# Performance work log

Hardware: AMD Instinct MI355X
Metric: run time of the kernel (lower is better)

The kernel has to match this reference:

```python
import jax, jax.numpy as jnp
import numpy as np

N_NODES = 100000
N_EDGES = 800000
F_IN, HID, N_CLS = 128, 512, 40
BN_EPS = 1e-5


def gcn_conv(x, W, b, src, dst, num_nodes):
    # PyG GCNConv: add self-loops, symmetric normalization.
    ones = jnp.ones(src.shape[0], x.dtype)
    deg = jax.ops.segment_sum(ones, dst, num_segments=num_nodes) + 1.0  # +1 self-loop
    dinv = jax.lax.rsqrt(deg)  # deg^-1/2, deg >= 1 so safe
    h = x @ W  # [N, out]
    norm = dinv[src] * dinv[dst]  # [E]
    agg = jax.ops.segment_sum(h[src] * norm[:, None], dst, num_segments=num_nodes)
    agg = agg + h * (dinv * dinv)[:, None]  # self-loop term: deg_i^-1 * h_i
    return agg + b


def batch_norm(x, gamma, beta):
    # training-mode BatchNorm over node axis (biased variance)
    mu = jnp.mean(x, axis=0)
    var = jnp.var(x, axis=0)
    return gamma * (x - mu) * jax.lax.rsqrt(var + BN_EPS) + beta


def setup_inputs() -> dict:
    key = jax.random.key(0)
    ks = jax.random.split(key, 12)
    x = jax.random.normal(ks[0], (N_NODES, F_IN), jnp.float32)
    edge_index = jax.random.randint(ks[1], (2, N_EDGES), 0, N_NODES, jnp.int64)
    def lin(k, fi, fo):
        s = 1.0 / np.sqrt(fi)
        return jax.random.uniform(k, (fi, fo), jnp.float32, -s, s)
    return {
        "x": x, "edge_index": edge_index,
        "W1": lin(ks[2], F_IN, HID), "b1": jnp.zeros((HID,), jnp.float32),
        "g1": jnp.ones((HID,), jnp.float32), "be1": jnp.zeros((HID,), jnp.float32),
        "W2": lin(ks[3], HID, HID), "b2": jnp.zeros((HID,), jnp.float32),
        "g2": jnp.ones((HID,), jnp.float32), "be2": jnp.zeros((HID,), jnp.float32),
        "W3": lin(ks[4], HID, N_CLS), "b3": jnp.zeros((N_CLS,), jnp.float32),
        "g3": jnp.ones((N_CLS,), jnp.float32), "be3": jnp.zeros((N_CLS,), jnp.float32),
    }


def reference(x, edge_index, W1, b1, g1, be1, W2, b2, g2, be2, W3, b3, g3, be3):
    src, dst = edge_index[0], edge_index[1]
    x1 = batch_norm(gcn_conv(x, W1, b1, src, dst, N_NODES), g1, be1)
    x3 = jax.nn.relu(x1)  # dropout is identity in eval mode
    x4 = batch_norm(gcn_conv(x3, W2, b2, src, dst, N_NODES), g2, be2)
    x6 = jax.nn.relu(x4)
    out = batch_norm(gcn_conv(x6, W3, b3, src, dst, N_NODES), g3, be3)
    return (out, x6)
```

## Files before the change

kernel.cpp:

```cpp
#include <hip/hip_runtime.h>
#include <cstddef>
#include <cstdint>


#define NN 100000
#define MPAD 100096
#define NE 800000
#define FIN 128
#define HIDD 512
#define NCLS 40
#define BN_EPS 1e-5f

typedef unsigned short ushort_t;
typedef __bf16 bf16x8_t __attribute__((ext_vector_type(8)));
typedef float f32x4_t __attribute__((ext_vector_type(4)));

static inline int ceil_div_ll(long long a, long long b) { return (int)((a + b - 1) / b); }

__device__ inline unsigned f2u(float f) { union { float f; unsigned u; } v; v.f = f; return v.u; }
__device__ inline float u2f(unsigned u) { union { unsigned u; float f; } v; v.u = u; return v.f; }
__device__ inline unsigned rne16(float f) {
    unsigned u = f2u(f);
    return (u + 0x7FFFu + ((u >> 16) & 1u)) >> 16;
}
__device__ inline unsigned pack2(float lo, float hi) { return rne16(lo) | (rne16(hi) << 16); }

__device__ inline void gld16(const void* g, void* l) {
    __builtin_amdgcn_global_load_lds(
        (const __attribute__((address_space(1))) unsigned int*)g,
        (__attribute__((address_space(3))) unsigned int*)l, 16, 0, 0);
}

__global__ void deg_int_kernel(const int* __restrict__ dst, int* __restrict__ degi) {
    int e = blockIdx.x * 256 + threadIdx.x;
    if (e < NE) atomicAdd(&degi[dst[e]], 1);
}

__global__ void dinv_from_deg_kernel(const int* __restrict__ degi, float* __restrict__ dinv) {
    int i = blockIdx.x * 256 + threadIdx.x;
    if (i < NN) dinv[i] = rsqrtf((float)degi[i] + 1.0f);
}

__global__ void scan_block_kernel(const int* __restrict__ degi, int* __restrict__ rowptr,
                                  int* __restrict__ bsum) {
    __shared__ int tmp[256];
    int t = threadIdx.x;
    int i = blockIdx.x * 256 + t;
    int v = (i < NN) ? degi[i] : 0;
    tmp[t] = v;
    __syncthreads();
    #pragma unroll
    for (int off = 1; off < 256; off <<= 1) {
        int u = (t >= off) ? tmp[t - off] : 0;
        __syncthreads();
        tmp[t] += u;
        __syncthreads();
    }
    if (i < NN) rowptr[i] = tmp[t] - v;
    if (t == 255) bsum[blockIdx.x] = tmp[255];
}

__global__ void scan_bsum_kernel(const int* __restrict__ bsum, int* __restrict__ boff, int nb) {
    __shared__ int tmp[512];
    int t = threadIdx.x;
    int v = (t < nb) ? bsum[t] : 0;
    tmp[t] = v;
    __syncthreads();
    #pragma unroll
    for (int off = 1; off < 512; off <<= 1) {
        int u = (t >= off) ? tmp[t - off] : 0;
        __syncthreads();
        tmp[t] += u;
        __syncthreads();
    }
    if (t < nb) boff[t] = tmp[t] - v;
}

__global__ void add_offsets_kernel(int* __restrict__ rowptr, const int* __restrict__ boff,
                                   int* __restrict__ cursor) {
    int i = blockIdx.x * 256 + threadIdx.x;
    if (i < NN) {
        int r = rowptr[i] + boff[i >> 8];
        rowptr[i] = r;
        cursor[i] = r;
    }
}

__global__ void scatter_kernel(const int* __restrict__ src, const int* __restrict__ dst,
                               const float* __restrict__ dinv, int* __restrict__ cursor,
                               int* __restrict__ csr_src, float* __restrict__ csr_w) {
    int e = blockIdx.x * 256 + threadIdx.x;
    if (e >= NE) return;
    int s = src[e];
    int d = dst[e];
    int pos = atomicAdd(&cursor[d], 1);
    csr_src[pos] = s;
    csr_w[pos] = dinv[s];
}

__global__ void f32_to_bf16_kernel(const float* __restrict__ X, unsigned* __restrict__ Y,
                                   long long n8) {
    long long i = (long long)blockIdx.x * 256 + threadIdx.x;
    if (i >= n8) return;
    const float4* X4 = reinterpret_cast<const float4*>(X);
    float4 a = X4[i * 2], b = X4[i * 2 + 1];
    uint4 o;
    o.x = pack2(a.x, a.y); o.y = pack2(a.z, a.w);
    o.z = pack2(b.x, b.y); o.w = pack2(b.z, b.w);
    reinterpret_cast<uint4*>(Y)[i] = o;
}

__global__ void transpose_w_kernel(const float* __restrict__ W, ushort_t* __restrict__ Wt,
                                   int K, int Nw, int Npad) {
    int gid = blockIdx.x * 256 + threadIdx.x;
    if (gid >= Npad * K) return;
    int k = gid % K;
    int n = gid / K;
    float v = (n < Nw) ? W[(size_t)k * Nw + n] : 0.0f;
    Wt[gid] = (ushort_t)rne16(v);
}

__global__ __launch_bounds__(256) void agg_csr512b_kernel(
        const ushort_t* __restrict__ h, const int* __restrict__ rowptr,
        const int* __restrict__ degi, const float* __restrict__ dinv,
        const int* __restrict__ csr_src, const float* __restrict__ csr_w,
        ushort_t* __restrict__ out) {
    int wid = (blockIdx.x * 256 + threadIdx.x) >> 6;
    int lane = threadIdx.x & 63;
    if (wid >= NN) return;
    int r0 = rowptr[wid];
    int n = degi[wid];
    float di = dinv[wid];
    float a[8] = {0.f, 0.f, 0.f, 0.f, 0.f, 0.f, 0.f, 0.f};
    for (int j = 0; j < n; ++j) {
        int s = csr_src[r0 + j];
        float w = csr_w[r0 + j];
        uint4 v = reinterpret_cast<const uint4*>(h + (size_t)s * HIDD)[lane];
        a[0] += w * u2f(v.x << 16); a[1] += w * u2f(v.x & 0xFFFF0000u);
        a[2] += w * u2f(v.y << 16); a[3] += w * u2f(v.y & 0xFFFF0000u);
        a[4] += w * u2f(v.z << 16); a[5] += w * u2f(v.z & 0xFFFF0000u);
        a[6] += w * u2f(v.w << 16); a[7] += w * u2f(v.w & 0xFFFF0000u);
    }
    uint4 sv = reinterpret_cast<const uint4*>(h + (size_t)wid * HIDD)[lane];
    float sq = di * di;
    float o[8];
    o[0] = di * a[0] + sq * u2f(sv.x << 16); o[1] = di * a[1] + sq * u2f(sv.x & 0xFFFF0000u);
    o[2] = di * a[2] + sq * u2f(sv.y << 16); o[3] = di * a[3] + sq * u2f(sv.y & 0xFFFF0000u);
    o[4] = di * a[4] + sq * u2f(sv.z << 16); o[5] = di * a[5] + sq * u2f(sv.z & 0xFFFF0000u);
    o[6] = di * a[6] + sq * u2f(sv.w << 16); o[7] = di * a[7] + sq * u2f(sv.w & 0xFFFF0000u);
    uint4 ov;
    ov.x = pack2(o[0], o[1]); ov.y = pack2(o[2], o[3]);
    ov.z = pack2(o[4], o[5]); ov.w = pack2(o[6], o[7]);
    reinterpret_cast<uint4*>(out + (size_t)wid * HIDD)[lane] = ov;
}

__global__ __launch_bounds__(256) void agg_csr128b_kernel(
        const ushort_t* __restrict__ h, const int* __restrict__ rowptr,
        const int* __restrict__ degi, const float* __restrict__ dinv,
        const int* __restrict__ csr_src, const float* __restrict__ csr_w,
        ushort_t* __restrict__ out) {
    int wid = (blockIdx.x * 256 + threadIdx.x) >> 6;
    int lane = threadIdx.x & 63;
    if (wid >= NN) return;
    int r0 = rowptr[wid];
    int n = degi[wid];
    float di = dinv[wid];
    float a0 = 0.f, a1 = 0.f;
    for (int j = 0; j < n; ++j) {
        int s = csr_src[r0 + j];
        float w = csr_w[r0 + j];
        unsigned v = reinterpret_cast<const unsigned*>(h + (size_t)s * FIN)[lane];
        a0 += w * u2f(v << 16);
        a1 += w * u2f(v & 0xFFFF0000u);
    }
    unsigned sv = reinterpret_cast<const unsigned*>(h + (size_t)wid * FIN)[lane];
    float sq = di * di;
    float o0 = di * a0 + sq * u2f(sv << 16);
    float o1 = di * a1 + sq * u2f(sv & 0xFFFF0000u);
    reinterpret_cast<unsigned*>(out + (size_t)wid * FIN)[lane] = pack2(o0, o1);
}

__global__ __launch_bounds__(256) void agg_csr40_kernel(
        const float* __restrict__ h, const int* __restrict__ rowptr,
        const int* __restrict__ degi, const float* __restrict__ dinv,
        const int* __restrict__ csr_src, const float* __restrict__ csr_w,
        float* __restrict__ out) {
    int wid = (blockIdx.x * 256 + threadIdx.x) >> 6;
    int lane = threadIdx.x & 63;
    if (wid >= NN) return;
    int r0 = rowptr[wid];
    int n = degi[wid];
    float di = dinv[wid];
    if (lane < 10) {
        float4 a = make_float4(0.f, 0.f, 0.f, 0.f);
        for (int j = 0; j < n; ++j) {
            int s = csr_src[r0 + j];
            float w = csr_w[r0 + j];
            float4 v = reinterpret_cast<const float4*>(h + (size_t)s * NCLS)[lane];
            a.x += w * v.x; a.y += w * v.y; a.z += w * v.z; a.w += w * v.w;
        }
        float4 sv = reinterpret_cast<const float4*>(h + (size_t)wid * NCLS)[lane];
        float sq = di * di;
        float4 o;
        o.x = di * a.x + sq * sv.x; o.y = di * a.y + sq * sv.y;
        o.z = di * a.z + sq * sv.z; o.w = di * a.w + sq * sv.w;
        reinterpret_cast<float4*>(out + (size_t)wid * NCLS)[lane] = o;
    }
}

template<int WM, int WN, int BNt, bool OUTBF>
__global__ __launch_bounds__(256) void gemm_bf16_kernel(
        const ushort_t* __restrict__ A, const ushort_t* __restrict__ Bt,
        void* __restrict__ C, int M, int N, int K, int ldc) {
    constexpr int BM = 128;
    constexpr int SM = BM / WM;
    constexpr int SN = BNt / WN;
    constexpr int MFR = SM / 16;
    constexpr int NFR = SN / 16;
    constexpr int AR = (BM * 128) / 4096;
    constexpr int BR = (BNt * 128) / 4096;

    __shared__ __align__(16) char smem[(BM + BNt) * 128];
    char* Asm = smem;
    char* Bsm = smem + BM * 128;

    const int tid = threadIdx.x;
    const int l = tid & 63;
    const int w = tid >> 6;
    const int wm = w / WN, wn = w % WN;
    const int m0 = blockIdx.y * BM;
    const int n0 = blockIdx.x * BNt;

    f32x4_t acc[MFR][NFR];
    #pragma unroll
    for (int mi = 0; mi < MFR; ++mi)
        #pragma unroll
        for (int ni = 0; ni < NFR; ++ni)
            acc[mi][ni] = (f32x4_t){0.f, 0.f, 0.f, 0.f};

    const int lrow = l >> 3;
    const int pchunk = l & 7;

    for (int k0 = 0; k0 < K; k0 += 64) {
        #pragma unroll
        for (int g = 0; g < AR; ++g) {
            int lr = g * 32 + w * 8 + lrow;
            int lchunk = pchunk ^ (lr & 7);
            gld16((const char*)A + ((size_t)(m0 + lr) * K + k0 + lchunk * 8) * 2,
                  Asm + (g * 32 + w * 8) * 128);
        }
        #pragma unroll
        for (int g = 0; g < BR; ++g) {
            int lr = g * 32 + w * 8 + lrow;
            int lchunk = pchunk ^ (lr & 7);
            gld16((const char*)Bt + ((size_t)(n0 + lr) * K + k0 + lchunk * 8) * 2,
                  Bsm + (g * 32 + w * 8) * 128);
        }
        __syncthreads();

        #pragma unroll
        for (int kk = 0; kk < 2; ++kk) {
            bf16x8_t af[MFR], bfr[NFR];
            #pragma unroll
            for (int mi = 0; mi < MFR; ++mi) {
                int ar = wm * SM + mi * 16 + (l & 15);
                int lchunk = (kk * 4 + (l >> 4)) ^ (ar & 7);
                af[mi] = *reinterpret_cast<const bf16x8_t*>(Asm + ar * 128 + lchunk * 16);
            }
            #pragma unroll
            for (int ni = 0; ni < NFR; ++ni) {
                int br = wn * SN + ni * 16 + (l & 15);
                int lchunk = (kk * 4 + (l >> 4)) ^ (br & 7);
                bfr[ni] = *reinterpret_cast<const bf16x8_t*>(Bsm + br * 128 + lchunk * 16);
            }
            #pragma unroll
            for (int mi = 0; mi < MFR; ++mi)
                #pragma unroll
                for (int ni = 0; ni < NFR; ++ni)
                    acc[mi][ni] = __builtin_amdgcn_mfma_f32_16x16x32_bf16(
                        af[mi], bfr[ni], acc[mi][ni], 0, 0, 0);
        }
        __syncthreads();
    }

    #pragma unroll
    for (int mi = 0; mi < MFR; ++mi) {
        #pragma unroll
        for (int r = 0; r < 4; ++r) {
            int row = m0 + wm * SM + mi * 16 + (l >> 4) * 4 + r;
            if (row >= M) continue;
            #pragma unroll
            for (int ni = 0; ni < NFR; ++ni) {
                int col = n0 + wn * SN + ni * 16 + (l & 15);
                if (col < N) {
                    float v = acc[mi][ni][r];
                    if (OUTBF)
                        ((ushort_t*)C)[(size_t)row * ldc + col] = (ushort_t)rne16(v);
                    else
                        ((float*)C)[(size_t)row * ldc + col] = v;
                }
            }
        }
    }
}

__global__ void colstats_bf16_kernel(const ushort_t* __restrict__ X, int C, int rows_per_block,
                                     float* __restrict__ colsum, float* __restrict__ colsumsq) {
    int col = blockIdx.y * 256 + threadIdx.x;
    if (col >= C) return;
    int r0 = blockIdx.x * rows_per_block;
    int r1 = min(r0 + rows_per_block, NN);
    float s = 0.f, ss = 0.f;
    for (int r = r0; r < r1; ++r) {
        float v = u2f(((unsigned)X[(size_t)r * C + col]) << 16);
        s += v;
        ss += v * v;
    }
    atomicAdd(&colsum[col], s);
    atomicAdd(&colsumsq[col], ss);
}

__global__ void colstats_f32_kernel(const float* __restrict__ X, int C, int rows_per_block,
                                    float* __restrict__ colsum, float* __restrict__ colsumsq) {
    int col = blockIdx.y * 256 + threadIdx.x;
    if (col >= C) return;
    int r0 = blockIdx.x * rows_per_block;
    int r1 = min(r0 + rows_per_block, NN);
    float s = 0.f, ss = 0.f;
    for (int r = r0; r < r1; ++r) {
        float v = X[(size_t)r * C + col];
        s += v;
        ss += v * v;
    }
    atomicAdd(&colsum[col], s);
    atomicAdd(&colsumsq[col], ss);
}

__global__ void finalize_stats_kernel(const float* __restrict__ colsum,
                                      const float* __restrict__ colsumsq,
                                      float* __restrict__ meanv, float* __restrict__ rstdv,
                                      int C) {
    int c = blockIdx.x * 256 + threadIdx.x;
    if (c >= C) return;
    float mu = colsum[c] * (1.0f / NN);
    float var = colsumsq[c] * (1.0f / NN) - mu * mu;
    meanv[c] = mu;
    rstdv[c] = rsqrtf(var + BN_EPS);
}

template<bool RELU>
__global__ void bn_bf16_kernel(ushort_t* __restrict__ Y, float* __restrict__ f32out,
                               const float* __restrict__ meanv, const float* __restrict__ rstdv,
                               const float* __restrict__ g, const float* __restrict__ be, int C) {
    long long i = (long long)blockIdx.x * 256 + threadIdx.x;
    long long tot = (long long)NN * (C / 8);
    if (i >= tot) return;
    int c0 = (int)(i % (C / 8)) * 8;
    uint4 v = reinterpret_cast<const uint4*>(Y)[i];
    float f[8];
    f[0] = u2f(v.x << 16); f[1] = u2f(v.x & 0xFFFF0000u);
    f[2] = u2f(v.y << 16); f[3] = u2f(v.y & 0xFFFF0000u);
    f[4] = u2f(v.z << 16); f[5] = u2f(v.z & 0xFFFF0000u);
    f[6] = u2f(v.w << 16); f[7] = u2f(v.w & 0xFFFF0000u);
    #pragma unroll
    for (int j = 0; j < 8; ++j) {
        float y = g[c0 + j] * (f[j] - meanv[c0 + j]) * rstdv[c0 + j] + be[c0 + j];
        if (RELU) y = fmaxf(y, 0.f);
        f[j] = y;
    }
    uint4 o;
    o.x = pack2(f[0], f[1]); o.y = pack2(f[2], f[3]);
    o.z = pack2(f[4], f[5]); o.w = pack2(f[6], f[7]);
    reinterpret_cast<uint4*>(Y)[i] = o;
    if (f32out) {
        long long row = i / (C / 8);
        float* p = f32out + row * C + c0;
        reinterpret_cast<float4*>(p)[0] = make_float4(f[0], f[1], f[2], f[3]);
        reinterpret_cast<float4*>(p)[1] = make_float4(f[4], f[5], f[6], f[7]);
    }
}

template<bool RELU, int C>
__global__ void bn_f32_kernel(const float* __restrict__ X, float* __restrict__ Y,
                              const float* __restrict__ meanv, const float* __restrict__ rstdv,
                              const float* __restrict__ g, const float* __restrict__ be) {
    const long long TOT = (long long)NN * (C / 4);
    long long i = (long long)blockIdx.x * 256 + threadIdx.x;
    if (i >= TOT) return;
    int c = (int)((i % (C / 4)) * 4);
    float4 v = reinterpret_cast<const float4*>(X)[i];
    float r[4] = {v.x, v.y, v.z, v.w};
    #pragma unroll
    for (int j = 0; j < 4; ++j) {
        float y = g[c + j] * (r[j] - meanv[c + j]) * rstdv[c + j] + be[c + j];
        if (RELU) y = fmaxf(y, 0.f);
        r[j] = y;
    }
    reinterpret_cast<float4*>(Y)[i] = make_float4(r[0], r[1], r[2], r[3]);
}

extern "C" void kernel_launch(void* const* d_in, const int* in_sizes, int n_in,
                              void* d_out, int out_size, void* d_ws, size_t ws_size,
                              hipStream_t stream) {
    const float* x   = (const float*)d_in[0];
    const int*   ei  = (const int*)d_in[1];
    const float* W1  = (const float*)d_in[2];
    const float* g1  = (const float*)d_in[4];
    const float* be1 = (const float*)d_in[5];
    const float* W2  = (const float*)d_in[6];
    const float* g2  = (const float*)d_in[8];
    const float* be2 = (const float*)d_in[9];
    const float* W3  = (const float*)d_in[10];
    const float* g3  = (const float*)d_in[12];
    const float* be3 = (const float*)d_in[13];

    const int* src = ei;
    const int* dst = ei + NE;

    float* out = (float*)d_out;
    float* x6  = out + (size_t)NN * NCLS;

    char* wp = (char*)d_ws;
    size_t o = 0;
    auto take = [&](size_t bytes) { char* p = wp + o; o = (o + bytes + 255) & ~(size_t)255; return p; };
    float*    dinv     = (float*)take((size_t)NN * 4);
    int*      degi     = (int*)take((size_t)NN * 4);
    int*      rowptr   = (int*)take((size_t)NN * 4);
    int*      cursor   = (int*)take((size_t)NN * 4);
    int*      bsum     = (int*)take(512 * 4);
    int*      boff     = (int*)take(512 * 4);
    float*    colsum   = (float*)take(512 * 4);
    float*    colsumsq = (float*)take(512 * 4);
    float*    meanv    = (float*)take(512 * 4);
    float*    rstdv    = (float*)take(512 * 4);
    int*      csr_src  = (int*)take((size_t)NE * 4);
    float*    csr_w    = (float*)take((size_t)NE * 4);
    ushort_t* W1t      = (ushort_t*)take((size_t)512 * 128 * 2);
    ushort_t* W2t      = (ushort_t*)take((size_t)512 * 512 * 2);
    ushort_t* W3t      = (ushort_t*)take((size_t)64 * 512 * 2);
    ushort_t* xb       = (ushort_t*)take((size_t)NN * FIN * 2);
    ushort_t* aggX1b   = (ushort_t*)take((size_t)MPAD * FIN * 2);
    ushort_t* y1b      = (ushort_t*)take((size_t)MPAD * HIDD * 2);
    ushort_t* aggX3b   = (ushort_t*)take((size_t)MPAD * HIDD * 2);
    ushort_t* y2b      = (ushort_t*)take((size_t)MPAD * HIDD * 2);
    float*    h3       = (float*)take((size_t)NN * NCLS * 4);
    float*    agg3     = (float*)take((size_t)NN * NCLS * 4);

    const int B = 256;
    const int NB = ceil_div_ll(NN, 256);

    hipMemsetAsync(degi, 0, (size_t)NN * 4, stream);
    deg_int_kernel<<<ceil_div_ll(NE, B), B, 0, stream>>>(dst, degi);
    dinv_from_deg_kernel<<<NB, B, 0, stream>>>(degi, dinv);
    scan_block_kernel<<<NB, B, 0, stream>>>(degi, rowptr, bsum);
    scan_bsum_kernel<<<1, 512, 0, stream>>>(bsum, boff, NB);
    add_offsets_kernel<<<NB, B, 0, stream>>>(rowptr, boff, cursor);
    scatter_kernel<<<ceil_div_ll(NE, B), B, 0, stream>>>(src, dst, dinv, cursor, csr_src, csr_w);

    transpose_w_kernel<<<ceil_div_ll(512 * 128, B), B, 0, stream>>>(W1, W1t, 128, 512, 512);
    transpose_w_kernel<<<ceil_div_ll(512 * 512, B), B, 0, stream>>>(W2, W2t, 512, 512, 512);
    transpose_w_kernel<<<ceil_div_ll(64 * 512, B), B, 0, stream>>>(W3, W3t, 512, 40, 64);
    f32_to_bf16_kernel<<<ceil_div_ll((long long)NN * FIN / 8, B), B, 0, stream>>>(
        x, (unsigned*)xb, (long long)NN * FIN / 8);

    const int MG = MPAD / 128;

    agg_csr128b_kernel<<<ceil_div_ll(NN, 4), B, 0, stream>>>(xb, rowptr, degi, dinv, csr_src, csr_w, aggX1b);
    {
        dim3 grid(HIDD / 128, MG);
        gemm_bf16_kernel<2, 2, 128, true><<<grid, B, 0, stream>>>(aggX1b, W1t, y1b, NN, HIDD, FIN, HIDD);
    }
    hipMemsetAsync(colsum, 0, 4096, stream);
    {
        dim3 grid(ceil_div_ll(NN, 128), 2);
        colstats_bf16_kernel<<<grid, B, 0, stream>>>(y1b, HIDD, 128, colsum, colsumsq);
    }
    finalize_stats_kernel<<<2, B, 0, stream>>>(colsum, colsumsq, meanv, rstdv, HIDD);
    bn_bf16_kernel<true><<<ceil_div_ll((long long)NN * HIDD / 8, B), B, 0, stream>>>(
        y1b, nullptr, meanv, rstdv, g1, be1, HIDD);

    agg_csr512b_kernel<<<ceil_div_ll(NN, 4), B, 0, stream>>>(y1b, rowptr, degi, dinv, csr_src, csr_w, aggX3b);
    {
        dim3 grid(HIDD / 128, MG);
        gemm_bf16_kernel<2, 2, 128, true><<<grid, B, 0, stream>>>(aggX3b, W2t, y2b, NN, HIDD, HIDD, HIDD);
    }
    hipMemsetAsync(colsum, 0, 4096, stream);
    {
        dim3 grid(ceil_div_ll(NN, 128), 2);
        colstats_bf16_kernel<<<grid, B, 0, stream>>>(y2b, HIDD, 128, colsum, colsumsq);
    }
    finalize_stats_kernel<<<2, B, 0, stream>>>(colsum, colsumsq, meanv, rstdv, HIDD);
    bn_bf16_kernel<true><<<ceil_div_ll((long long)NN * HIDD / 8, B), B, 0, stream>>>(
        y2b, x6, meanv, rstdv, g2, be2, HIDD);

    {
        dim3 grid(1, MG);
        gemm_bf16_kernel<4, 1, 64, false><<<grid, B, 0, stream>>>(y2b, W3t, h3, NN, NCLS, HIDD, NCLS);
    }
    agg_csr40_kernel<<<ceil_div_ll(NN, 4), B, 0, stream>>>(h3, rowptr, degi, dinv, csr_src, csr_w, agg3);
    hipMemsetAsync(colsum, 0, 4096, stream);
    {
        dim3 grid(ceil_div_ll(NN, 128), 1);
        colstats_f32_kernel<<<grid, B, 0, stream>>>(agg3, NCLS, 128, colsum, colsumsq);
    }
    finalize_stats_kernel<<<1, B, 0, stream>>>(colsum, colsumsq, meanv, rstdv, NCLS);
    bn_f32_kernel<false, NCLS><<<ceil_div_ll((long long)NN * NCLS / 4, B), B, 0, stream>>>(
        agg3, out, meanv, rstdv, g3, be3);
}
```

Measured before the change: 1.123 ms.

## Fuse BN column stats into GEMM epilogue and BN+ReLU into aggregation

Column sum and sum-of-squares are computed in the GEMM epilogue with warp shuffles and shared-memory atomics, replacing separate colstats passes. Layer-1 batchnorm and ReLU are applied on the fly inside the 512-wide aggregation kernel, removing the standalone BN pass over y1. Aggregation loops are unrolled by two for more memory-level parallelism. Padded GEMM rows are zeroed so they add nothing to the stats. In exchange, BN math is recomputed for every gathered neighbor, and the epilogue adds atomics.

```diff
diff --git a/kernel.cpp b/kernel.cpp
--- a/kernel.cpp
+++ b/kernel.cpp
@@ -120,34 +120,67 @@
     Wt[gid] = (ushort_t)rne16(v);
 }
 
-__global__ __launch_bounds__(256) void agg_csr512b_kernel(
+__global__ __launch_bounds__(256) void agg_bn512_kernel(
         const ushort_t* __restrict__ h, const int* __restrict__ rowptr,
         const int* __restrict__ degi, const float* __restrict__ dinv,
         const int* __restrict__ csr_src, const float* __restrict__ csr_w,
+        const float* __restrict__ meanv, const float* __restrict__ rstdv,
+        const float* __restrict__ g, const float* __restrict__ be,
         ushort_t* __restrict__ out) {
     int wid = (blockIdx.x * 256 + threadIdx.x) >> 6;
     int lane = threadIdx.x & 63;
     if (wid >= NN) return;
+    const int c0 = lane * 8;
+    float sc[8], sh[8];
+    #pragma unroll
+    for (int j = 0; j < 8; ++j) {
+        float s = g[c0 + j] * rstdv[c0 + j];
+        sc[j] = s;
+        sh[j] = be[c0 + j] - meanv[c0 + j] * s;
+    }
     int r0 = rowptr[wid];
     int n = degi[wid];
     float di = dinv[wid];
     float a[8] = {0.f, 0.f, 0.f, 0.f, 0.f, 0.f, 0.f, 0.f};
-    for (int j = 0; j < n; ++j) {
-        int s = csr_src[r0 + j];
-        float w = csr_w[r0 + j];
-        uint4 v = reinterpret_cast<const uint4*>(h + (size_t)s * HIDD)[lane];
-        a[0] += w * u2f(v.x << 16); a[1] += w * u2f(v.x & 0xFFFF0000u);
-        a[2] += w * u2f(v.y << 16); a[3] += w * u2f(v.y & 0xFFFF0000u);
-        a[4] += w * u2f(v.z << 16); a[5] += w * u2f(v.z & 0xFFFF0000u);
-        a[6] += w * u2f(v.w << 16); a[7] += w * u2f(v.w & 0xFFFF0000u);
-    }
+
+    auto accum = [&](uint4 v, float w) {
+        float f[8];
+        f[0] = u2f(v.x << 16); f[1] = u2f(v.x & 0xFFFF0000u);
+        f[2] = u2f(v.y << 16); f[3] = u2f(v.y & 0xFFFF0000u);
+        f[4] = u2f(v.z << 16); f[5] = u2f(v.z & 0xFFFF0000u);
+        f[6] = u2f(v.w << 16); f[7] = u2f(v.w & 0xFFFF0000u);
+        #pragma unroll
+        for (int j = 0; j < 8; ++j)
+            a[j] += w * fmaxf(sc[j] * f[j] + sh[j], 0.f);
+    };
+
+    int j = 0;
+    for (; j + 2 <= n; j += 2) {
+        int s0 = csr_src[r0 + j], s1 = csr_src[r0 + j + 1];
+        float w0 = csr_w[r0 + j], w1 = csr_w[r0 + j + 1];
+        uint4 v0 = reinterpret_cast<const uint4*>(h + (size_t)s0 * HIDD)[lane];
+        uint4 v1 = reinterpret_cast<const uint4*>(h + (size_t)s1 * HIDD)[lane];
+        accum(v0, w0);
+        accum(v1, w1);
+    }
+    if (j < n) {
+        int s0 = csr_src[r0 + j];
+        float w0 = csr_w[r0 + j];
+        uint4 v0 = reinterpret_cast<const uint4*>(h + (size_t)s0 * HIDD)[lane];
+        accum(v0, w0);
+    }
+
     uint4 sv = reinterpret_cast<const uint4*>(h + (size_t)wid * HIDD)[lane];
+    float fs[8];
+    fs[0] = u2f(sv.x << 16); fs[1] = u2f(sv.x & 0xFFFF0000u);
+    fs[2] = u2f(sv.y << 16); fs[3] = u2f(sv.y & 0xFFFF0000u);
+    fs[4] = u2f(sv.z << 16); fs[5] = u2f(sv.z & 0xFFFF0000u);
+    fs[6] = u2f(sv.w << 16); fs[7] = u2f(sv.w & 0xFFFF0000u);
     float sq = di * di;
     float o[8];
-    o[0] = di * a[0] + sq * u2f(sv.x << 16); o[1] = di * a[1] + sq * u2f(sv.x & 0xFFFF0000u);
-    o[2] = di * a[2] + sq * u2f(sv.y << 16); o[3] = di * a[3] + sq * u2f(sv.y & 0xFFFF0000u);
-    o[4] = di * a[4] + sq * u2f(sv.z << 16); o[5] = di * a[5] + sq * u2f(sv.z & 0xFFFF0000u);
-    o[6] = di * a[6] + sq * u2f(sv.w << 16); o[7] = di * a[7] + sq * u2f(sv.w & 0xFFFF0000u);
+    #pragma unroll
+    for (int jj = 0; jj < 8; ++jj)
+        o[jj] = di * a[jj] + sq * fmaxf(sc[jj] * fs[jj] + sh[jj], 0.f);
     uint4 ov;
     ov.x = pack2(o[0], o[1]); ov.y = pack2(o[2], o[3]);
     ov.z = pack2(o[4], o[5]); ov.w = pack2(o[6], o[7]);
@@ -166,12 +199,21 @@
     int n = degi[wid];
     float di = dinv[wid];
     float a0 = 0.f, a1 = 0.f;
-    for (int j = 0; j < n; ++j) {
-        int s = csr_src[r0 + j];
-        float w = csr_w[r0 + j];
-        unsigned v = reinterpret_cast<const unsigned*>(h + (size_t)s * FIN)[lane];
-        a0 += w * u2f(v << 16);
-        a1 += w * u2f(v & 0xFFFF0000u);
+    int j = 0;
+    for (; j + 2 <= n; j += 2) {
+        int s0 = csr_src[r0 + j], s1 = csr_src[r0 + j + 1];
+        float w0 = csr_w[r0 + j], w1 = csr_w[r0 + j + 1];
+        unsigned v0 = reinterpret_cast<const unsigned*>(h + (size_t)s0 * FIN)[lane];
+        unsigned v1 = reinterpret_cast<const unsigned*>(h + (size_t)s1 * FIN)[lane];
+        a0 += w0 * u2f(v0 << 16) + w1 * u2f(v1 << 16);
+        a1 += w0 * u2f(v0 & 0xFFFF0000u) + w1 * u2f(v1 & 0xFFFF0000u);
+    }
+    if (j < n) {
+        int s0 = csr_src[r0 + j];
+        float w0 = csr_w[r0 + j];
+        unsigned v0 = reinterpret_cast<const unsigned*>(h + (size_t)s0 * FIN)[lane];
+        a0 += w0 * u2f(v0 << 16);
+        a1 += w0 * u2f(v0 & 0xFFFF0000u);
     }
     unsigned sv = reinterpret_cast<const unsigned*>(h + (size_t)wid * FIN)[lane];
     float sq = di * di;
@@ -208,10 +250,11 @@
     }
 }
 
-template<int WM, int WN, int BNt, bool OUTBF>
+template<int WM, int WN, int BNt, bool OUTBF, bool STATS>
 __global__ __launch_bounds__(256) void gemm_bf16_kernel(
         const ushort_t* __restrict__ A, const ushort_t* __restrict__ Bt,
-        void* __restrict__ C, int M, int N, int K, int ldc) {
+        void* __restrict__ C, int M, int N, int K, int ldc,
+        float* __restrict__ colsum, float* __restrict__ colsumsq) {
     constexpr int BM = 128;
     constexpr int SM = BM / WM;
     constexpr int SN = BNt / WN;
@@ -302,22 +345,37 @@
             }
         }
     }
-}
-
-__global__ void colstats_bf16_kernel(const ushort_t* __restrict__ X, int C, int rows_per_block,
-                                     float* __restrict__ colsum, float* __restrict__ colsumsq) {
-    int col = blockIdx.y * 256 + threadIdx.x;
-    if (col >= C) return;
-    int r0 = blockIdx.x * rows_per_block;
-    int r1 = min(r0 + rows_per_block, NN);
-    float s = 0.f, ss = 0.f;
-    for (int r = r0; r < r1; ++r) {
-        float v = u2f(((unsigned)X[(size_t)r * C + col]) << 16);
-        s += v;
-        ss += v * v;
-    }
-    atomicAdd(&colsum[col], s);
-    atomicAdd(&colsumsq[col], ss);
+
+    if (STATS) {
+        float* sSum = (float*)smem;
+        float* sSq = sSum + BNt;
+        for (int i = tid; i < 2 * BNt; i += 256) sSum[i] = 0.f;
+        __syncthreads();
+        #pragma unroll
+        for (int ni = 0; ni < NFR; ++ni) {
+            float s = 0.f, q = 0.f;
+            #pragma unroll
+            for (int mi = 0; mi < MFR; ++mi)
+                #pragma unroll
+                for (int r = 0; r < 4; ++r) {
+                    float v = acc[mi][ni][r];
+                    s += v;
+                    q += v * v;
+                }
+            s += __shfl_xor(s, 16, 64); q += __shfl_xor(q, 16, 64);
+            s += __shfl_xor(s, 32, 64); q += __shfl_xor(q, 32, 64);
+            if ((l >> 4) == 0) {
+                int c = wn * SN + ni * 16 + (l & 15);
+                atomicAdd(&sSum[c], s);
+                atomicAdd(&sSq[c], q);
+            }
+        }
+        __syncthreads();
+        if (tid < BNt) {
+            atomicAdd(&colsum[n0 + tid], sSum[tid]);
+            atomicAdd(&colsumsq[n0 + tid], sSq[tid]);
+        }
+    }
 }
 
 __global__ void colstats_f32_kernel(const float* __restrict__ X, int C, int rows_per_block,
@@ -448,6 +506,7 @@
 
     const int B = 256;
     const int NB = ceil_div_ll(NN, 256);
+    const int MG = MPAD / 128;
 
     hipMemsetAsync(degi, 0, (size_t)NN * 4, stream);
     deg_int_kernel<<<ceil_div_ll(NE, B), B, 0, stream>>>(dst, degi);
@@ -462,32 +521,25 @@
     transpose_w_kernel<<<ceil_div_ll(64 * 512, B), B, 0, stream>>>(W3, W3t, 512, 40, 64);
     f32_to_bf16_kernel<<<ceil_div_ll((long long)NN * FIN / 8, B), B, 0, stream>>>(
         x, (unsigned*)xb, (long long)NN * FIN / 8);
-
-    const int MG = MPAD / 128;
+    hipMemsetAsync(aggX1b + (size_t)NN * FIN, 0, (size_t)(MPAD - NN) * FIN * 2, stream);
+    hipMemsetAsync(aggX3b + (size_t)NN * HIDD, 0, (size_t)(MPAD - NN) * HIDD * 2, stream);
 
     agg_csr128b_kernel<<<ceil_div_ll(NN, 4), B, 0, stream>>>(xb, rowptr, degi, dinv, csr_src, csr_w, aggX1b);
+    hipMemsetAsync(colsum, 0, 4096, stream);
     {
         dim3 grid(HIDD / 128, MG);
-        gemm_bf16_kernel<2, 2, 128, true><<<grid, B, 0, stream>>>(aggX1b, W1t, y1b, NN, HIDD, FIN, HIDD);
-    }
+        gemm_bf16_kernel<2, 2, 128, true, true><<<grid, B, 0, stream>>>(
+            aggX1b, W1t, y1b, NN, HIDD, FIN, HIDD, colsum, colsumsq);
+    }
+    finalize_stats_kernel<<<2, B, 0, stream>>>(colsum, colsumsq, meanv, rstdv, HIDD);
+
+    agg_bn512_kernel<<<ceil_div_ll(NN, 4), B, 0, stream>>>(
+        y1b, rowptr, degi, dinv, csr_src, csr_w, meanv, rstdv, g1, be1, aggX3b);
     hipMemsetAsync(colsum, 0, 4096, stream);
     {
-        dim3 grid(ceil_div_ll(NN, 128), 2);
-        colstats_bf16_kernel<<<grid, B, 0, stream>>>(y1b, HIDD, 128, colsum, colsumsq);
-    }
-    finalize_stats_kernel<<<2, B, 0, stream>>>(colsum, colsumsq, meanv, rstdv, HIDD);
-    bn_bf16_kernel<true><<<ceil_div_ll((long long)NN * HIDD / 8, B), B, 0, stream>>>(
-        y1b, nullptr, meanv, rstdv, g1, be1, HIDD);
-
-    agg_csr512b_kernel<<<ceil_div_ll(NN, 4), B, 0, stream>>>(y1b, rowptr, degi, dinv, csr_src, csr_w, aggX3b);
-    {
         dim3 grid(HIDD / 128, MG);
-        gemm_bf16_kernel<2, 2, 128, true><<<grid, B, 0, stream>>>(aggX3b, W2t, y2b, NN, HIDD, HIDD, HIDD);
-    }
-    hipMemsetAsync(colsum, 0, 4096, stream);
-    {
-        dim3 grid(ceil_div_ll(NN, 128), 2);
-        colstats_bf16_kernel<<<grid, B, 0, stream>>>(y2b, HIDD, 128, colsum, colsumsq);
+        gemm_bf16_kernel<2, 2, 128, true, true><<<grid, B, 0, stream>>>(
+            aggX3b, W2t, y2b, NN, HIDD, HIDD, HIDD, colsum, colsumsq);
     }
     finalize_stats_kernel<<<2, B, 0, stream>>>(colsum, colsumsq, meanv, rstdv, HIDD);
     bn_bf16_kernel<true><<<ceil_div_ll((long long)NN * HIDD / 8, B), B, 0, stream>>>(
@@ -495,7 +547,8 @@
 
     {
         dim3 grid(1, MG);
-        gemm_bf16_kernel<4, 1, 64, false><<<grid, B, 0, stream>>>(y2b, W3t, h3, NN, NCLS, HIDD, NCLS);
+        gemm_bf16_kernel<4, 1, 64, false, false><<<grid, B, 0, stream>>>(
+            y2b, W3t, h3, NN, NCLS, HIDD, NCLS, nullptr, nullptr);
     }
     agg_csr40_kernel<<<ceil_div_ll(NN, 4), B, 0, stream>>>(h3, rowptr, degi, dinv, csr_src, csr_w, agg3);
     hipMemsetAsync(colsum, 0, 4096, stream);
```

After: 985.1 us. -12.3%, faster.
